# Optimization experiments

Hardware: AMD Instinct MI355X
Metric: run time of the kernel (lower is better)

## Reference

```python
import jax, jax.numpy as jnp
import numpy as np

B, SEQ, D_MODEL, N_HEADS = 4, 4096, 1024, 16
HEAD_DIM = D_MODEL // N_HEADS


def setup_inputs() -> dict:
    key = jax.random.key(0)
    ks = jax.random.split(key, 12)
    d = D_MODEL
    s = 1.0 / np.sqrt(d)  # ~nn.Linear init scale
    f = lambda k, shape, sc=1.0: jax.random.normal(k, shape, dtype=jnp.float32) * sc
    return {
        "queries": f(ks[0], (B, SEQ, d)),
        "keys":    f(ks[1], (B, SEQ, d)),
        "values":  f(ks[2], (B, SEQ, d)),
        "Wr": f(ks[3], (d, d), s), "br": jnp.zeros((d,), jnp.float32),
        "Wk": f(ks[4], (d, d), s), "bk": jnp.zeros((d,), jnp.float32),
        "Wv": f(ks[5], (d, d), s), "bv": jnp.zeros((d,), jnp.float32),
        "Wo": f(ks[6], (d, d), s), "bo": jnp.zeros((d,), jnp.float32),
        "decay": f(ks[7], (N_HEADS, HEAD_DIM), 0.01) - 5.0,
        "bonus": jnp.zeros((N_HEADS, HEAD_DIM), jnp.float32),
    }


def reference(queries, keys, values, Wr, br, Wk, bk, Wv, bv, Wo, bo, decay, bonus):
    Bb, N, d = queries.shape
    M = keys.shape[1]
    H = decay.shape[0]
    Dh = d // H

    # projections (nn.Linear: x @ W^T + b), split into heads
    r = (queries @ Wr.T + br).reshape(Bb, N, H, Dh)              # (B,N,H,D)
    k = (keys    @ Wk.T + bk).reshape(Bb, M, H, Dh).transpose(1, 0, 2, 3)  # (M,B,H,D)
    v = (values  @ Wv.T + bv).reshape(Bb, M, H, Dh).transpose(1, 0, 2, 3)  # (M,B,H,D)

    decay_factor = jnp.exp(-jnp.exp(decay))  # exp(w), w = -exp(decay); (H,D)

    def step(carry, kv):
        num, den = carry                       # (B,H,D)
        k_t, v_t = kv                          # (B,H,D)
        kc = jnp.clip(k_t, -10.0, 10.0)
        ek = jnp.exp(kc)
        bonus_w = jnp.exp(bonus + kc)          # (B,H,D) via broadcast
        wkv_t = (num + bonus_w * v_t) / (den + bonus_w + 1e-6)
        num = num * decay_factor + ek * v_t
        den = den * decay_factor + ek
        return (num, den), wkv_t

    init = (jnp.zeros((Bb, H, Dh), queries.dtype), jnp.zeros((Bb, H, Dh), queries.dtype))
    _, wkv = jax.lax.scan(step, init, (k, v))   # (M,B,H,D); here M == N
    wkv = wkv[:N].transpose(1, 0, 2, 3)         # (B,N,H,D)

    out = (jax.nn.sigmoid(r) * wkv).reshape(Bb, N, d)
    return out @ Wo.T + bo
```

## Files before the change

### kernel.cpp

```cpp
#include <hip/hip_runtime.h>

#define T_SEQ   4096
#define DM      1024
#define NB      4
#define ROWS    (NB * T_SEQ)
#define NCH     64
#define LCH     (T_SEQ / NCH)

typedef unsigned short ushort_t;

typedef __attribute__((ext_vector_type(8))) short bf16x8;
typedef __attribute__((ext_vector_type(4))) float f32x4;

__device__ __forceinline__ float bf2f(ushort_t u) {
  return __uint_as_float(((unsigned int)u) << 16);
}
__device__ __forceinline__ ushort_t f2bf(float f) {
  unsigned int u = __float_as_uint(f);
  u += 0x7FFFu + ((u >> 16) & 1u);
  return (ushort_t)(u >> 16);
}
__device__ __forceinline__ unsigned cvtpk(float lo, float hi) {
  unsigned r;
  asm("v_cvt_pk_bf16_f32 %0, %1, %2" : "=v"(r) : "v"(lo), "v"(hi));
  return r;
}

__device__ __forceinline__ void async16(const void* g, void* l) {
  __builtin_amdgcn_global_load_lds(
      (const __attribute__((address_space(1))) unsigned int*)g,
      (__attribute__((address_space(3))) unsigned int*)l, 16, 0, 0);
}

__device__ __forceinline__ int fragoff(int row, int col) {
  int p = (((row >> 4) * 2 + (col >> 5)) << 10) + ((row & 15) << 6) + ((col & 31) << 1);
  return p ^ (((row >> 3) & 1) << 5);
}
__device__ __forceinline__ int fragoffB32(int row, int col) {
  int p = ((row >> 4) << 10) + ((row & 15) << 6) + (col << 1);
  return p ^ (((row >> 3) & 1) << 5);
}
__device__ __forceinline__ int fragoffA32f(int row, int col) {
  int p = ((row >> 3) << 10) + ((row & 7) << 7) + (col << 2);
  return p ^ ((row & 7) << 4);
}

__global__ __launch_bounds__(256)
void cvt_pack(const float* __restrict__ Wr, const float* __restrict__ Wk,
              const float* __restrict__ Wv, const float* __restrict__ Wo,
              const float* __restrict__ br, const float* __restrict__ bk,
              const float* __restrict__ bv, const float* __restrict__ bo,
              ushort_t* __restrict__ wb, float* __restrict__ biasP) {
  const int bid = blockIdx.x;
  if (bid < 2048) {
    const int n4 = (DM * DM);
    for (int i = bid * 256 + threadIdx.x; i < n4; i += 2048 * 256) {
      const int seg = i >> 18;
      const float* src = seg == 0 ? Wr : seg == 1 ? Wk : seg == 2 ? Wv : Wo;
      const float4 f = ((const float4*)src)[i & 262143];
      ushort4 o;
      o.x = f2bf(f.x); o.y = f2bf(f.y); o.z = f2bf(f.z); o.w = f2bf(f.w);
      ((ushort4*)wb)[i] = o;
    }
  } else {
    const int s = bid - 2048;
    const float* b = s == 0 ? br : s == 1 ? bk : s == 2 ? bv : bo;
    for (int i = threadIdx.x; i < DM; i += 256) biasP[s * DM + i] = b[i];
  }
}

template <typename OutT>
__global__ __launch_bounds__(512, 2)
void gemm256(const ushort_t* __restrict__ A, const ushort_t* __restrict__ W,
             const float* __restrict__ bias, OutT* __restrict__ C,
             const int M, const int N, const int K) {
  __shared__ char smem[131072];
  const int T = K >> 6;
  const int nwg = (M >> 8) * (N >> 8);
  const int wg  = ((int)blockIdx.x & 7) * (nwg >> 3) + ((int)blockIdx.x >> 3);
  const int ntn = N >> 8;
  const int tm = wg / ntn, tn = wg % ntn;
  const int m0 = tm << 8, n0 = tn << 8;
  const int tid  = threadIdx.x;
  const int lane = tid & 63;
  const int wave = tid >> 6;
  const int wm128 = (wave >> 2) * 128;
  const int wn64  = (wave & 3) * 64;
  const int r15 = lane & 15;
  const int kq8 = (lane >> 4) * 8;

  int srow[2], scol[2];
  #pragma unroll
  for (int rho = 0; rho < 2; ++rho) {
    int p  = rho * 8192 + tid * 16;
    int pp = p ^ (((p >> 9) & 1) << 5);
    int e  = pp >> 1;
    int S = e >> 9, inr = e & 511;
    srow[rho] = ((S >> 1) << 4) + (inr >> 5);
    scol[rho] = ((S & 1) << 5) + (inr & 31);
  }

  auto stageA = [&](int tile, int half) {
    const int boff = ((tile & 1) << 15) + (half << 14);
    #pragma unroll
    for (int rho = 0; rho < 2; ++rho) {
      const ushort_t* g = A + (size_t)(m0 + half * 128 + srow[rho]) * K + (tile << 6) + scol[rho];
      async16(g, &smem[boff + rho * 8192 + tid * 16]);
    }
  };
  auto stageB = [&](int tile, int half) {
    const int boff = 65536 + ((tile & 1) << 15) + (half << 14);
    #pragma unroll
    for (int rho = 0; rho < 2; ++rho) {
      const ushort_t* g = W + (size_t)(n0 + half * 128 + srow[rho]) * K + (tile << 6) + scol[rho];
      async16(g, &smem[boff + rho * 8192 + tid * 16]);
    }
  };

  f32x4 acc[8][4];
  #pragma unroll
  for (int i = 0; i < 8; ++i)
    #pragma unroll
    for (int j = 0; j < 4; ++j)
      acc[i][j] = (f32x4){0.f, 0.f, 0.f, 0.f};
  bf16x8 bf[4][2];

  stageA(0, 0); stageA(0, 1); stageB(0, 0); stageB(0, 1); stageB(1, 0); stageB(1, 1);
  asm volatile("s_waitcnt vmcnt(4)" ::: "memory");
  __builtin_amdgcn_s_barrier();

#define GPHASE(Q, STG, TAILW)                                                    \
  {                                                                              \
    bf16x8 af[2][2];                                                             \
    _Pragma("unroll") for (int fl = 0; fl < 2; ++fl)                             \
      _Pragma("unroll") for (int ks = 0; ks < 2; ++ks)                           \
        af[fl][ks] = *(const bf16x8*)&smem[abase +                               \
            fragoff(wm128 + ((2 * (Q) + fl) << 4) + r15, (ks << 5) + kq8)];      \
    if ((Q) == 0) {                                                              \
      _Pragma("unroll") for (int fj = 0; fj < 4; ++fj)                           \
        _Pragma("unroll") for (int ks = 0; ks < 2; ++ks)                         \
          bf[fj][ks] = *(const bf16x8*)&smem[bbase +                             \
              fragoff(wn64 + (fj << 4) + r15, (ks << 5) + kq8)];                 \
    }                                                                            \
    STG();                                                                       \
    __builtin_amdgcn_s_barrier();                                                \
    __builtin_amdgcn_s_setprio(1);                                               \
    _Pragma("unroll") for (int fl = 0; fl < 2; ++fl)                             \
      _Pragma("unroll") for (int fj = 0; fj < 4; ++fj)                           \
        _Pragma("unroll") for (int ks = 0; ks < 2; ++ks)                         \
          acc[2 * (Q) + fl][fj] = __builtin_amdgcn_mfma_f32_16x16x32_bf16(       \
              af[fl][ks], bf[fj][ks], acc[2 * (Q) + fl][fj], 0, 0, 0);           \
    __builtin_amdgcn_s_setprio(0);                                               \
    TAILW();                                                                     \
    __builtin_amdgcn_s_barrier();                                                \
  }

  for (int j = 0; j < T; ++j) {
    const int abase = (j & 1) << 15;
    const int bbase = 65536 + ((j & 1) << 15);
    const bool p1 = (j + 1 < T), p2 = (j + 2 < T);
    auto s0 = [&] { if (p1) stageA(j + 1, 0); };
    auto s1 = [&] { if (p1) stageA(j + 1, 1); };
    auto s2 = [&] { if (p2) stageB(j + 2, 0); };
    auto s3 = [&] { if (p2) stageB(j + 2, 1); };
    auto nw = [&] {};
    auto bwait = [&] {
      if (p2) asm volatile("s_waitcnt vmcnt(4)" ::: "memory");
      else    asm volatile("s_waitcnt vmcnt(0)" ::: "memory");
    };
    GPHASE(0, s0, nw);
    GPHASE(1, s1, nw);
    GPHASE(2, s2, nw);
    GPHASE(3, s3, bwait);
  }
#undef GPHASE

  float bias4[4];
  #pragma unroll
  for (int fj = 0; fj < 4; ++fj) bias4[fj] = bias[n0 + wn64 + fj * 16 + r15];
  #pragma unroll
  for (int fi = 0; fi < 8; ++fi) {
    const int row0 = m0 + wm128 + fi * 16 + (lane >> 4) * 4;
    #pragma unroll
    for (int fj = 0; fj < 4; ++fj) {
      const int col = n0 + wn64 + fj * 16 + r15;
      #pragma unroll
      for (int r = 0; r < 4; ++r) {
        const float v = acc[fi][fj][r] + bias4[fj];
        if constexpr (sizeof(OutT) == 2) C[(size_t)(row0 + r) * N + col] = f2bf(v);
        else                             C[(size_t)(row0 + r) * N + col] = v;
      }
    }
  }
}

__global__ __launch_bounds__(512, 2)
void gemm256_proj(const float* __restrict__ Aq, const float* __restrict__ Ak,
                  const float* __restrict__ Av, const ushort_t* __restrict__ Wb,
                  const float* __restrict__ biasP, ushort_t* __restrict__ Cb,
                  const int M, const int N, const int K) {
  __shared__ char smem[98304];
  const int T = K >> 5;
  const int wg = ((int)blockIdx.x & 7) * 96 + ((int)blockIdx.x >> 3);
  const int g  = wg >> 8;
  const int local = wg & 255;
  const int ntn = N >> 8;
  const int tm = local / ntn, tn = local % ntn;
  const int m0 = tm << 8, n0 = tn << 8;
  const float*    Af = g == 0 ? Aq : (g == 1 ? Ak : Av);
  const ushort_t* W  = Wb + (size_t)g * N * K;
  const float*  bias = biasP + g * N;
  ushort_t*        C = Cb + (size_t)g * M * N;

  const int tid  = threadIdx.x;
  const int lane = tid & 63;
  const int wave = tid >> 6;
  const int wm128 = (wave >> 2) * 128;
  const int wn64  = (wave & 3) * 64;
  const int r15 = lane & 15;
  const int kq8 = (lane >> 4) * 8;

  int arow[2], acol[2];
  #pragma unroll
  for (int rho = 0; rho < 2; ++rho) {
    const int p = rho * 8192 + tid * 16;
    const int e = p ^ (((p >> 7) & 7) << 4);
    arow[rho] = ((p >> 10) << 3) | ((p >> 7) & 7);
    acol[rho] = (e >> 2) & 31;
  }
  int brow, bcol;
  {
    const int p = tid * 16;
    const int pp = p ^ (((p >> 9) & 1) << 5);
    const int e = pp >> 1;
    brow = ((e >> 9) << 4) | ((e >> 5) & 15);
    bcol = e & 31;
  }

  auto stageA = [&](int tile, int half) {
    const int boff = ((tile & 1) << 15) + (half << 14);
    #pragma unroll
    for (int rho = 0; rho < 2; ++rho) {
      const float* g2 = Af + (size_t)(m0 + half * 128 + arow[rho]) * K + (tile << 5) + acol[rho];
      async16(g2, &smem[boff + rho * 8192 + tid * 16]);
    }
  };
  auto stageB = [&](int tile, int half) {
    const int boff = 65536 + ((tile & 1) << 14) + (half << 13);
    const ushort_t* g2 = W + (size_t)(n0 + half * 128 + brow) * K + (tile << 5) + bcol;
    async16(g2, &smem[boff + tid * 16]);
  };

  auto rdA = [&](int abase, int row) -> bf16x8 {
    const int adlo = abase + fragoffA32f(row, kq8);
    const int adhi = abase + fragoffA32f(row, kq8 + 4);
    const f32x4 lo = *(const f32x4*)&smem[adlo];
    const f32x4 hi = *(const f32x4*)&smem[adhi];
    union { uint4 u4; bf16x8 b; } cv;
    cv.u4.x = cvtpk(lo[0], lo[1]); cv.u4.y = cvtpk(lo[2], lo[3]);
    cv.u4.z = cvtpk(hi[0], hi[1]); cv.u4.w = cvtpk(hi[2], hi[3]);
    return cv.b;
  };

  f32x4 acc[8][4];
  #pragma unroll
  for (int i = 0; i < 8; ++i)
    #pragma unroll
    for (int j = 0; j < 4; ++j)
      acc[i][j] = (f32x4){0.f, 0.f, 0.f, 0.f};
  bf16x8 bf[4];

  stageA(0, 0); stageA(0, 1); stageB(0, 0); stageB(0, 1); stageB(1, 0); stageB(1, 1);
  asm volatile("s_waitcnt vmcnt(2)" ::: "memory");
  __builtin_amdgcn_s_barrier();

#define PPHASE(Q, STG, TAILW)                                                    \
  {                                                                              \
    bf16x8 af[2];                                                                \
    _Pragma("unroll") for (int fl = 0; fl < 2; ++fl)                             \
      af[fl] = rdA(abase, wm128 + ((2 * (Q) + fl) << 4) + r15);                  \
    if ((Q) == 0) {                                                              \
      _Pragma("unroll") for (int fj = 0; fj < 4; ++fj)                           \
        bf[fj] = *(const bf16x8*)&smem[bbase +                                   \
            fragoffB32(wn64 + (fj << 4) + r15, kq8)];                            \
    }                                                                            \
    STG();                                                                       \
    __builtin_amdgcn_s_barrier();                                                \
    __builtin_amdgcn_s_setprio(1);                                               \
    _Pragma("unroll") for (int fl = 0; fl < 2; ++fl)                             \
      _Pragma("unroll") for (int fj = 0; fj < 4; ++fj)                           \
        acc[2 * (Q) + fl][fj] = __builtin_amdgcn_mfma_f32_16x16x32_bf16(         \
            af[fl], bf[fj], acc[2 * (Q) + fl][fj], 0, 0, 0);                     \
    __builtin_amdgcn_s_setprio(0);                                               \
    TAILW();                                                                     \
    __builtin_amdgcn_s_barrier();                                                \
  }

  for (int j = 0; j < T; ++j) {
    const int abase = (j & 1) << 15;
    const int bbase = 65536 + ((j & 1) << 14);
    const bool p1 = (j + 1 < T), p2 = (j + 2 < T);
    auto s0 = [&] { if (p1) stageA(j + 1, 0); };
    auto s1 = [&] { if (p1) stageA(j + 1, 1); };
    auto s2 = [&] { if (p2) { stageB(j + 2, 0); stageB(j + 2, 1); } };
    auto nw = [&] {};
    auto bwait = [&] {
      if (p2) asm volatile("s_waitcnt vmcnt(2)" ::: "memory");
      else    asm volatile("s_waitcnt vmcnt(0)" ::: "memory");
    };
    PPHASE(0, s0, nw);
    PPHASE(1, s1, nw);
    PPHASE(2, s2, nw);
    PPHASE(3, nw, bwait);
  }
#undef PPHASE

  float bias4[4];
  #pragma unroll
  for (int fj = 0; fj < 4; ++fj) bias4[fj] = bias[n0 + wn64 + fj * 16 + r15];
  #pragma unroll
  for (int fi = 0; fi < 8; ++fi) {
    const int row0 = m0 + wm128 + fi * 16 + (lane >> 4) * 4;
    #pragma unroll
    for (int fj = 0; fj < 4; ++fj) {
      const int col = n0 + wn64 + fj * 16 + r15;
      #pragma unroll
      for (int r = 0; r < 4; ++r)
        C[(size_t)(row0 + r) * N + col] = f2bf(acc[fi][fj][r] + bias4[fj]);
    }
  }
}

__global__ __launch_bounds__(256)
void wkv_pass1(const ushort_t* __restrict__ kp, const ushort_t* __restrict__ vp,
               const float* __restrict__ decay,
               float* __restrict__ s_num, float* __restrict__ s_den) {
  const int tid = threadIdx.x;
  const int grp = blockIdx.x & 3;
  const int c   = (blockIdx.x >> 2) & (NCH - 1);
  const int b   = (int)blockIdx.x >> 8;
  const int ch  = grp * 256 + tid;
  const float df = __expf(-__expf(decay[ch]));
  size_t idx = (size_t)b * T_SEQ * DM + (size_t)(c * LCH) * DM + ch;
  float num = 0.f, den = 0.f;
  for (int u = 0; u < LCH; ++u, idx += DM) {
    float kf = bf2f(kp[idx]);
    kf = fminf(fmaxf(kf, -10.f), 10.f);
    const float ek = __expf(kf);
    const float vv = bf2f(vp[idx]);
    num = fmaf(num, df, ek * vv);
    den = fmaf(den, df, ek);
  }
  const size_t si = ((size_t)b * NCH + c) * DM + ch;
  s_num[si] = num;
  s_den[si] = den;
}

__global__ __launch_bounds__(256)
void wkv_pass2(const float* __restrict__ decay,
               float* __restrict__ s_num, float* __restrict__ s_den) {
  const int tid = threadIdx.x;
  const int grp = blockIdx.x & 3;
  const int b   = (int)blockIdx.x >> 2;
  const int ch  = grp * 256 + tid;
  const float dfL = __expf(-__expf(decay[ch]) * (float)LCH);
  float an = 0.f, ad = 0.f;
  size_t si = (size_t)b * NCH * DM + ch;
  for (int c = 0; c < NCH; ++c, si += DM) {
    const float ln = s_num[si], ld = s_den[si];
    s_num[si] = an; s_den[si] = ad;
    an = fmaf(an, dfL, ln);
    ad = fmaf(ad, dfL, ld);
  }
}

__global__ __launch_bounds__(256)
void wkv_pass3(const ushort_t* __restrict__ kp, const ushort_t* __restrict__ vp,
               ushort_t* rg, const float* __restrict__ decay,
               const float* __restrict__ bonus,
               const float* __restrict__ s_num, const float* __restrict__ s_den) {
  const int tid = threadIdx.x;
  const int grp = blockIdx.x & 3;
  const int c   = (blockIdx.x >> 2) & (NCH - 1);
  const int b   = (int)blockIdx.x >> 8;
  const int ch  = grp * 256 + tid;
  const float df = __expf(-__expf(decay[ch]));
  const float eb = __expf(bonus[ch]);
  const size_t si = ((size_t)b * NCH + c) * DM + ch;
  float num = s_num[si], den = s_den[si];
  size_t idx = (size_t)b * T_SEQ * DM + (size_t)(c * LCH) * DM + ch;
  for (int u = 0; u < LCH; ++u, idx += DM) {
    float kf = bf2f(kp[idx]);
    kf = fminf(fmaxf(kf, -10.f), 10.f);
    const float ek = __expf(kf);
    const float bw = eb * ek;
    const float vv = bf2f(vp[idx]);
    const float rr = bf2f(rg[idx]);
    const float numer = fmaf(bw, vv, num);
    const float denom = den + bw + 1e-6f;
    const float wkv = numer * __builtin_amdgcn_rcpf(denom);
    const float sig = __builtin_amdgcn_rcpf(1.f + __expf(-rr));
    rg[idx] = f2bf(sig * wkv);
    num = fmaf(num, df, ek * vv);
    den = fmaf(den, df, ek);
  }
}

extern "C" void kernel_launch(void* const* d_in, const int* in_sizes, int n_in,
                              void* d_out, int out_size, void* d_ws, size_t ws_size,
                              hipStream_t stream) {
  const float* q   = (const float*)d_in[0];
  const float* ky  = (const float*)d_in[1];
  const float* vl  = (const float*)d_in[2];
  const float* Wr  = (const float*)d_in[3];
  const float* br  = (const float*)d_in[4];
  const float* Wk  = (const float*)d_in[5];
  const float* bk  = (const float*)d_in[6];
  const float* Wv  = (const float*)d_in[7];
  const float* bv  = (const float*)d_in[8];
  const float* Wo  = (const float*)d_in[9];
  const float* bo  = (const float*)d_in[10];
  const float* decay = (const float*)d_in[11];
  const float* bonus = (const float*)d_in[12];
  float* out = (float*)d_out;

  const size_t NE = (size_t)ROWS * DM;
  const size_t WE = (size_t)DM * DM;

  ushort_t* wb = (ushort_t*)d_ws;
  float* biasP = (float*)(wb + 4 * WE);
  ushort_t* rp = (ushort_t*)(biasP + 4 * DM);
  ushort_t* kp = rp + NE;
  ushort_t* vp = kp + NE;
  float* s_num = (float*)(vp + NE);
  float* s_den = s_num + (size_t)NB * NCH * DM;
  ushort_t* G  = rp;

  dim3 cB(256);
  dim3 gemmGrid((ROWS / 256) * (DM / 256)), gemmBlk(512);
  dim3 projGrid(3 * (ROWS / 256) * (DM / 256));
  dim3 scanGrid(NB * NCH * (DM / 256)), scanBlk(256);

  cvt_pack<<<dim3(2052), cB, 0, stream>>>(Wr, Wk, Wv, Wo, br, bk, bv, bo, wb, biasP);
  gemm256_proj<<<projGrid, gemmBlk, 0, stream>>>(q, ky, vl, wb, biasP, rp, ROWS, DM, DM);
  wkv_pass1<<<scanGrid, scanBlk, 0, stream>>>(kp, vp, decay, s_num, s_den);
  wkv_pass2<<<dim3(NB * DM / 256), scanBlk, 0, stream>>>(decay, s_num, s_den);
  wkv_pass3<<<scanGrid, scanBlk, 0, stream>>>(kp, vp, rp, decay, bonus, s_num, s_den);
  gemm256<float><<<gemmGrid, gemmBlk, 0, stream>>>(G, wb + 3 * WE, biasP + 3 * DM, out, ROWS, DM, DM);
}
```

Before: 258.8 us.

## Restructure projection GEMM with triple-buffered A and 64-wide K B tiles

```diff
diff --git a/kernel.cpp b/kernel.cpp
--- a/kernel.cpp
+++ b/kernel.cpp
@@ -35,14 +35,6 @@
 __device__ __forceinline__ int fragoff(int row, int col) {
   int p = (((row >> 4) * 2 + (col >> 5)) << 10) + ((row & 15) << 6) + ((col & 31) << 1);
   return p ^ (((row >> 3) & 1) << 5);
-}
-__device__ __forceinline__ int fragoffB32(int row, int col) {
-  int p = ((row >> 4) << 10) + ((row & 15) << 6) + (col << 1);
-  return p ^ (((row >> 3) & 1) << 5);
-}
-__device__ __forceinline__ int fragoffA32f(int row, int col) {
-  int p = ((row >> 3) << 10) + ((row & 7) << 7) + (col << 2);
-  return p ^ ((row & 7) << 4);
 }
 
 __global__ __launch_bounds__(256)
@@ -195,22 +187,24 @@
 }
 
 __global__ __launch_bounds__(512, 2)
-void gemm256_proj(const float* __restrict__ Aq, const float* __restrict__ Ak,
-                  const float* __restrict__ Av, const ushort_t* __restrict__ Wb,
-                  const float* __restrict__ biasP, ushort_t* __restrict__ Cb,
-                  const int M, const int N, const int K) {
-  __shared__ char smem[98304];
+void gemm3p(const float* __restrict__ Aq, const float* __restrict__ Ak,
+            const float* __restrict__ Av, const ushort_t* __restrict__ Wb,
+            const float* __restrict__ biasP, ushort_t* __restrict__ Cb,
+            const int M, const int N, const int K) {
+  __shared__ char smem[163840];
   const int T = K >> 5;
-  const int wg = ((int)blockIdx.x & 7) * 96 + ((int)blockIdx.x >> 3);
-  const int g  = wg >> 8;
-  const int local = wg & 255;
+  const int ntpg = (M >> 8) * (N >> 8);
+  const int nwg  = 3 * ntpg;
+  const int wg = ((int)blockIdx.x & 7) * (nwg >> 3) + ((int)blockIdx.x >> 3);
+  const int g     = wg / ntpg;
+  const int local = wg % ntpg;
   const int ntn = N >> 8;
   const int tm = local / ntn, tn = local % ntn;
   const int m0 = tm << 8, n0 = tn << 8;
-  const float*    Af = g == 0 ? Aq : (g == 1 ? Ak : Av);
-  const ushort_t* W  = Wb + (size_t)g * N * K;
-  const float*  bias = biasP + g * N;
-  ushort_t*        C = Cb + (size_t)g * M * N;
+  const float*    Af   = g == 0 ? Aq : (g == 1 ? Ak : Av);
+  const ushort_t* W    = Wb + (size_t)g * N * K;
+  const float*    bias = biasP + g * N;
+  ushort_t*       C    = Cb + (size_t)g * M * N;
 
   const int tid  = threadIdx.x;
   const int lane = tid & 63;
@@ -220,42 +214,47 @@
   const int r15 = lane & 15;
   const int kq8 = (lane >> 4) * 8;
 
-  int arow[2], acol[2];
+  int arow[4], acol[4];
+  #pragma unroll
+  for (int rho = 0; rho < 4; ++rho) {
+    const int p = (rho & 1) * 8192 + tid * 16;
+    const int e = (p ^ (((p >> 9) & 1) << 5)) >> 1;
+    const int S = e >> 9, inr = e & 511;
+    const int srl = ((S >> 1) << 4) + (inr >> 5);
+    const int E   = ((S & 1) << 5) + (inr & 31);
+    arow[rho] = (rho >> 1) * 128 + srl;
+    acol[rho] = ((E & 31) >> 3) * 8 + (E >> 5) * 4;
+  }
+  int brow[2], bcolE[2];
   #pragma unroll
   for (int rho = 0; rho < 2; ++rho) {
     const int p = rho * 8192 + tid * 16;
-    const int e = p ^ (((p >> 7) & 7) << 4);
-    arow[rho] = ((p >> 10) << 3) | ((p >> 7) & 7);
-    acol[rho] = (e >> 2) & 31;
-  }
-  int brow, bcol;
-  {
-    const int p = tid * 16;
-    const int pp = p ^ (((p >> 9) & 1) << 5);
-    const int e = pp >> 1;
-    brow = ((e >> 9) << 4) | ((e >> 5) & 15);
-    bcol = e & 31;
-  }
-
-  auto stageA = [&](int tile, int half) {
-    const int boff = ((tile & 1) << 15) + (half << 14);
+    const int e = (p ^ (((p >> 9) & 1) << 5)) >> 1;
+    const int S = e >> 9, inr = e & 511;
+    brow[rho]  = ((S >> 1) << 4) + (inr >> 5);
+    bcolE[rho] = ((S & 1) << 5) + (inr & 31);
+  }
+
+  auto stageA = [&](int tile) {
+    const int boff = (tile % 3) * 32768;
+    #pragma unroll
+    for (int rho = 0; rho < 4; ++rho) {
+      const float* s = Af + (size_t)(m0 + arow[rho]) * K + (tile << 5) + acol[rho];
+      async16(s, &smem[boff + (rho >> 1) * 16384 + (rho & 1) * 8192 + tid * 16]);
+    }
+  };
+  auto stageBh = [&](int bt, int half) {
+    const int boff = 98304 + (bt & 1) * 32768 + half * 16384;
     #pragma unroll
     for (int rho = 0; rho < 2; ++rho) {
-      const float* g2 = Af + (size_t)(m0 + half * 128 + arow[rho]) * K + (tile << 5) + acol[rho];
-      async16(g2, &smem[boff + rho * 8192 + tid * 16]);
+      const ushort_t* s = W + (size_t)(n0 + half * 128 + brow[rho]) * K + (bt << 6) + bcolE[rho];
+      async16(s, &smem[boff + rho * 8192 + tid * 16]);
     }
   };
-  auto stageB = [&](int tile, int half) {
-    const int boff = 65536 + ((tile & 1) << 14) + (half << 13);
-    const ushort_t* g2 = W + (size_t)(n0 + half * 128 + brow) * K + (tile << 5) + bcol;
-    async16(g2, &smem[boff + tid * 16]);
-  };
 
   auto rdA = [&](int abase, int row) -> bf16x8 {
-    const int adlo = abase + fragoffA32f(row, kq8);
-    const int adhi = abase + fragoffA32f(row, kq8 + 4);
-    const f32x4 lo = *(const f32x4*)&smem[adlo];
-    const f32x4 hi = *(const f32x4*)&smem[adhi];
+    const f32x4 lo = *(const f32x4*)&smem[abase + fragoff(row, kq8)];
+    const f32x4 hi = *(const f32x4*)&smem[abase + fragoff(row, kq8 + 32)];
     union { uint4 u4; bf16x8 b; } cv;
     cv.u4.x = cvtpk(lo[0], lo[1]); cv.u4.y = cvtpk(lo[2], lo[3]);
     cv.u4.z = cvtpk(hi[0], hi[1]); cv.u4.w = cvtpk(hi[2], hi[3]);
@@ -268,52 +267,58 @@
     #pragma unroll
     for (int j = 0; j < 4; ++j)
       acc[i][j] = (f32x4){0.f, 0.f, 0.f, 0.f};
-  bf16x8 bf[4];
-
-  stageA(0, 0); stageA(0, 1); stageB(0, 0); stageB(0, 1); stageB(1, 0); stageB(1, 1);
-  asm volatile("s_waitcnt vmcnt(2)" ::: "memory");
+  bf16x8 bfr[4];
+
+  stageA(0); stageBh(0, 0); stageBh(0, 1); stageA(1);
+  asm volatile("s_waitcnt vmcnt(4)" ::: "memory");
   __builtin_amdgcn_s_barrier();
 
-#define PPHASE(Q, STG, TAILW)                                                    \
-  {                                                                              \
-    bf16x8 af[2];                                                                \
-    _Pragma("unroll") for (int fl = 0; fl < 2; ++fl)                             \
-      af[fl] = rdA(abase, wm128 + ((2 * (Q) + fl) << 4) + r15);                  \
-    if ((Q) == 0) {                                                              \
-      _Pragma("unroll") for (int fj = 0; fj < 4; ++fj)                           \
-        bf[fj] = *(const bf16x8*)&smem[bbase +                                   \
-            fragoffB32(wn64 + (fj << 4) + r15, kq8)];                            \
-    }                                                                            \
-    STG();                                                                       \
-    __builtin_amdgcn_s_barrier();                                                \
-    __builtin_amdgcn_s_setprio(1);                                               \
-    _Pragma("unroll") for (int fl = 0; fl < 2; ++fl)                             \
-      _Pragma("unroll") for (int fj = 0; fj < 4; ++fj)                           \
-        acc[2 * (Q) + fl][fj] = __builtin_amdgcn_mfma_f32_16x16x32_bf16(         \
-            af[fl], bf[fj], acc[2 * (Q) + fl][fj], 0, 0, 0);                     \
-    __builtin_amdgcn_s_setprio(0);                                               \
-    TAILW();                                                                     \
-    __builtin_amdgcn_s_barrier();                                                \
-  }
-
   for (int j = 0; j < T; ++j) {
-    const int abase = (j & 1) << 15;
-    const int bbase = 65536 + ((j & 1) << 14);
-    const bool p1 = (j + 1 < T), p2 = (j + 2 < T);
-    auto s0 = [&] { if (p1) stageA(j + 1, 0); };
-    auto s1 = [&] { if (p1) stageA(j + 1, 1); };
-    auto s2 = [&] { if (p2) { stageB(j + 2, 0); stageB(j + 2, 1); } };
-    auto nw = [&] {};
-    auto bwait = [&] {
-      if (p2) asm volatile("s_waitcnt vmcnt(2)" ::: "memory");
-      else    asm volatile("s_waitcnt vmcnt(0)" ::: "memory");
-    };
-    PPHASE(0, s0, nw);
-    PPHASE(1, s1, nw);
-    PPHASE(2, s2, nw);
-    PPHASE(3, nw, bwait);
-  }
-#undef PPHASE
+    const int curA = (j % 3) * 32768;
+    const int curB = 98304 + ((j >> 1) & 1) * 32768;
+    const int ks   = (j & 1) << 5;
+    const bool pre  = (j + 2 < T);
+    const bool even = !(j & 1);
+    {
+      bf16x8 af[4];
+      #pragma unroll
+      for (int q = 0; q < 4; ++q) af[q] = rdA(curA, wm128 + q * 16 + r15);
+      #pragma unroll
+      for (int fj = 0; fj < 4; ++fj)
+        bfr[fj] = *(const bf16x8*)&smem[curB + fragoff(wn64 + (fj << 4) + r15, ks + kq8)];
+      if (pre) { stageA(j + 2); if (even) stageBh((j >> 1) + 1, 0); }
+      __builtin_amdgcn_s_barrier();
+      __builtin_amdgcn_s_setprio(1);
+      #pragma unroll
+      for (int q = 0; q < 4; ++q)
+        #pragma unroll
+        for (int fj = 0; fj < 4; ++fj)
+          acc[q][fj] = __builtin_amdgcn_mfma_f32_16x16x32_bf16(af[q], bfr[fj], acc[q][fj], 0, 0, 0);
+      __builtin_amdgcn_s_setprio(0);
+      __builtin_amdgcn_s_barrier();
+    }
+    {
+      bf16x8 af[4];
+      #pragma unroll
+      for (int q = 0; q < 4; ++q) af[q] = rdA(curA, wm128 + 64 + q * 16 + r15);
+      if (pre && even) stageBh((j >> 1) + 1, 1);
+      __builtin_amdgcn_s_barrier();
+      __builtin_amdgcn_s_setprio(1);
+      #pragma unroll
+      for (int q = 0; q < 4; ++q)
+        #pragma unroll
+        for (int fj = 0; fj < 4; ++fj)
+          acc[4 + q][fj] = __builtin_amdgcn_mfma_f32_16x16x32_bf16(af[q], bfr[fj], acc[4 + q][fj], 0, 0, 0);
+      __builtin_amdgcn_s_setprio(0);
+      if (pre) {
+        if (even) asm volatile("s_waitcnt vmcnt(8)" ::: "memory");
+        else      asm volatile("s_waitcnt vmcnt(4)" ::: "memory");
+      } else if (j + 1 < T) {
+        asm volatile("s_waitcnt vmcnt(0)" ::: "memory");
+      }
+      __builtin_amdgcn_s_barrier();
+    }
+  }
 
   float bias4[4];
   #pragma unroll
@@ -437,12 +442,13 @@
   ushort_t* G  = rp;
 
   dim3 cB(256);
-  dim3 gemmGrid((ROWS / 256) * (DM / 256)), gemmBlk(512);
+  dim3 gemmBlk(512);
   dim3 projGrid(3 * (ROWS / 256) * (DM / 256));
+  dim3 gemmGrid((ROWS / 256) * (DM / 256));
   dim3 scanGrid(NB * NCH * (DM / 256)), scanBlk(256);
 
   cvt_pack<<<dim3(2052), cB, 0, stream>>>(Wr, Wk, Wv, Wo, br, bk, bv, bo, wb, biasP);
-  gemm256_proj<<<projGrid, gemmBlk, 0, stream>>>(q, ky, vl, wb, biasP, rp, ROWS, DM, DM);
+  gemm3p<<<projGrid, gemmBlk, 0, stream>>>(q, ky, vl, wb, biasP, rp, ROWS, DM, DM);
   wkv_pass1<<<scanGrid, scanBlk, 0, stream>>>(kp, vp, decay, s_num, s_den);
   wkv_pass2<<<dim3(NB * DM / 256), scanBlk, 0, stream>>>(decay, s_num, s_den);
   wkv_pass3<<<scanGrid, scanBlk, 0, stream>>>(kp, vp, rp, decay, bonus, s_num, s_den);
```

Result: no change. 263.9 us (+2.0%).

## Stage fp32 activations through registers with bf16 conversion before LDS in projection GEMM

Applied to the files above, without the earlier changes.

```diff
diff --git a/kernel.cpp b/kernel.cpp
--- a/kernel.cpp
+++ b/kernel.cpp
@@ -35,14 +35,6 @@
 __device__ __forceinline__ int fragoff(int row, int col) {
   int p = (((row >> 4) * 2 + (col >> 5)) << 10) + ((row & 15) << 6) + ((col & 31) << 1);
   return p ^ (((row >> 3) & 1) << 5);
-}
-__device__ __forceinline__ int fragoffB32(int row, int col) {
-  int p = ((row >> 4) << 10) + ((row & 15) << 6) + (col << 1);
-  return p ^ (((row >> 3) & 1) << 5);
-}
-__device__ __forceinline__ int fragoffA32f(int row, int col) {
-  int p = ((row >> 3) << 10) + ((row & 7) << 7) + (col << 2);
-  return p ^ ((row & 7) << 4);
 }
 
 __global__ __launch_bounds__(256)
@@ -195,22 +187,24 @@
 }
 
 __global__ __launch_bounds__(512, 2)
-void gemm256_proj(const float* __restrict__ Aq, const float* __restrict__ Ak,
-                  const float* __restrict__ Av, const ushort_t* __restrict__ Wb,
-                  const float* __restrict__ biasP, ushort_t* __restrict__ Cb,
-                  const int M, const int N, const int K) {
-  __shared__ char smem[98304];
-  const int T = K >> 5;
-  const int wg = ((int)blockIdx.x & 7) * 96 + ((int)blockIdx.x >> 3);
-  const int g  = wg >> 8;
-  const int local = wg & 255;
+void gemm3r(const float* __restrict__ Aq, const float* __restrict__ Ak,
+            const float* __restrict__ Av, const ushort_t* __restrict__ Wb,
+            const float* __restrict__ biasP, ushort_t* __restrict__ Cb,
+            const int M, const int N, const int K) {
+  __shared__ char smem[131072];
+  const int T = K >> 6;
+  const int ntpg = (M >> 8) * (N >> 8);
+  const int nwg  = 3 * ntpg;
+  const int wg = ((int)blockIdx.x & 7) * (nwg >> 3) + ((int)blockIdx.x >> 3);
+  const int g     = wg / ntpg;
+  const int local = wg % ntpg;
   const int ntn = N >> 8;
   const int tm = local / ntn, tn = local % ntn;
   const int m0 = tm << 8, n0 = tn << 8;
-  const float*    Af = g == 0 ? Aq : (g == 1 ? Ak : Av);
-  const ushort_t* W  = Wb + (size_t)g * N * K;
-  const float*  bias = biasP + g * N;
-  ushort_t*        C = Cb + (size_t)g * M * N;
+  const float*    Af   = g == 0 ? Aq : (g == 1 ? Ak : Av);
+  const ushort_t* W    = Wb + (size_t)g * N * K;
+  const float*    bias = biasP + g * N;
+  ushort_t*       C    = Cb + (size_t)g * M * N;
 
   const int tid  = threadIdx.x;
   const int lane = tid & 63;
@@ -220,47 +214,50 @@
   const int r15 = lane & 15;
   const int kq8 = (lane >> 4) * 8;
 
-  int arow[2], acol[2];
+  int srow[2], scol[2];
   #pragma unroll
   for (int rho = 0; rho < 2; ++rho) {
-    const int p = rho * 8192 + tid * 16;
-    const int e = p ^ (((p >> 7) & 7) << 4);
-    arow[rho] = ((p >> 10) << 3) | ((p >> 7) & 7);
-    acol[rho] = (e >> 2) & 31;
-  }
-  int brow, bcol;
-  {
-    const int p = tid * 16;
-    const int pp = p ^ (((p >> 9) & 1) << 5);
-    const int e = pp >> 1;
-    brow = ((e >> 9) << 4) | ((e >> 5) & 15);
-    bcol = e & 31;
-  }
-
-  auto stageA = [&](int tile, int half) {
-    const int boff = ((tile & 1) << 15) + (half << 14);
+    int p  = rho * 8192 + tid * 16;
+    int pp = p ^ (((p >> 9) & 1) << 5);
+    int e  = pp >> 1;
+    int S = e >> 9, inr = e & 511;
+    srow[rho] = ((S >> 1) << 4) + (inr >> 5);
+    scol[rho] = ((S & 1) << 5) + (inr & 31);
+  }
+  int aRow[4], aCol[4];
+  #pragma unroll
+  for (int s = 0; s < 4; ++s) {
+    aRow[s] = (s >> 1) * 128 + srow[s & 1];
+    aCol[s] = scol[s & 1];
+  }
+
+  auto stageB = [&](int tile, int half) {
+    const int boff = 65536 + ((tile & 1) << 15) + (half << 14);
     #pragma unroll
     for (int rho = 0; rho < 2; ++rho) {
-      const float* g2 = Af + (size_t)(m0 + half * 128 + arow[rho]) * K + (tile << 5) + acol[rho];
-      async16(g2, &smem[boff + rho * 8192 + tid * 16]);
+      const ushort_t* gq = W + (size_t)(n0 + half * 128 + srow[rho]) * K + (tile << 6) + scol[rho];
+      async16(gq, &smem[boff + rho * 8192 + tid * 16]);
     }
   };
-  auto stageB = [&](int tile, int half) {
-    const int boff = 65536 + ((tile & 1) << 14) + (half << 13);
-    const ushort_t* g2 = W + (size_t)(n0 + half * 128 + brow) * K + (tile << 5) + bcol;
-    async16(g2, &smem[boff + tid * 16]);
-  };
-
-  auto rdA = [&](int abase, int row) -> bf16x8 {
-    const int adlo = abase + fragoffA32f(row, kq8);
-    const int adhi = abase + fragoffA32f(row, kq8 + 4);
-    const f32x4 lo = *(const f32x4*)&smem[adlo];
-    const f32x4 hi = *(const f32x4*)&smem[adhi];
-    union { uint4 u4; bf16x8 b; } cv;
-    cv.u4.x = cvtpk(lo[0], lo[1]); cv.u4.y = cvtpk(lo[2], lo[3]);
-    cv.u4.z = cvtpk(hi[0], hi[1]); cv.u4.w = cvtpk(hi[2], hi[3]);
-    return cv.b;
-  };
+
+  float4 regE[8], regO[8];
+
+#define ALOAD(DST, TILE)                                                         \
+  _Pragma("unroll") for (int s = 0; s < 4; ++s) {                                \
+    const float* src_ = Af + (size_t)(m0 + aRow[s]) * K + ((TILE) << 6) + aCol[s]; \
+    DST[2 * s]     = *(const float4*)src_;                                       \
+    DST[2 * s + 1] = *(const float4*)(src_ + 4);                                 \
+  }
+#define AWRITE2(SRC, TILE, S0)                                                   \
+  _Pragma("unroll") for (int s = (S0); s < (S0) + 2; ++s) {                      \
+    uint4 w_;                                                                    \
+    w_.x = cvtpk(SRC[2 * s][0], SRC[2 * s][1]);                                  \
+    w_.y = cvtpk(SRC[2 * s][2], SRC[2 * s][3]);                                  \
+    w_.z = cvtpk(SRC[2 * s + 1][0], SRC[2 * s + 1][1]);                          \
+    w_.w = cvtpk(SRC[2 * s + 1][2], SRC[2 * s + 1][3]);                          \
+    *(uint4*)&smem[(((TILE) & 1) << 15) + (s >> 1) * 16384 + (s & 1) * 8192 +    \
+                   tid * 16] = w_;                                               \
+  }
 
   f32x4 acc[8][4];
   #pragma unroll
@@ -268,52 +265,67 @@
     #pragma unroll
     for (int j = 0; j < 4; ++j)
       acc[i][j] = (f32x4){0.f, 0.f, 0.f, 0.f};
-  bf16x8 bf[4];
-
-  stageA(0, 0); stageA(0, 1); stageB(0, 0); stageB(0, 1); stageB(1, 0); stageB(1, 1);
-  asm volatile("s_waitcnt vmcnt(2)" ::: "memory");
+  bf16x8 bf[4][2];
+
+  ALOAD(regE, 0);
+  stageB(0, 0); stageB(0, 1);
+  ALOAD(regO, 1);
+  stageB(1, 0); stageB(1, 1);
+  AWRITE2(regE, 0, 0); AWRITE2(regE, 0, 2);
+  asm volatile("s_waitcnt vmcnt(12)" ::: "memory");
+  asm volatile("s_waitcnt lgkmcnt(0)" ::: "memory");
   __builtin_amdgcn_s_barrier();
 
-#define PPHASE(Q, STG, TAILW)                                                    \
+#define RPHASE(Q, STG, TAILW)                                                    \
   {                                                                              \
-    bf16x8 af[2];                                                                \
+    bf16x8 af[2][2];                                                             \
     _Pragma("unroll") for (int fl = 0; fl < 2; ++fl)                             \
-      af[fl] = rdA(abase, wm128 + ((2 * (Q) + fl) << 4) + r15);                  \
+      _Pragma("unroll") for (int ks = 0; ks < 2; ++ks)                           \
+        af[fl][ks] = *(const bf16x8*)&smem[abase +                               \
+            fragoff(wm128 + ((2 * (Q) + fl) << 4) + r15, (ks << 5) + kq8)];      \
     if ((Q) == 0) {                                                              \
       _Pragma("unroll") for (int fj = 0; fj < 4; ++fj)                           \
-        bf[fj] = *(const bf16x8*)&smem[bbase +                                   \
-            fragoffB32(wn64 + (fj << 4) + r15, kq8)];                            \
+        _Pragma("unroll") for (int ks = 0; ks < 2; ++ks)                         \
+          bf[fj][ks] = *(const bf16x8*)&smem[bbase +                             \
+              fragoff(wn64 + (fj << 4) + r15, (ks << 5) + kq8)];                 \
     }                                                                            \
-    STG();                                                                       \
+    STG                                                                          \
     __builtin_amdgcn_s_barrier();                                                \
     __builtin_amdgcn_s_setprio(1);                                               \
     _Pragma("unroll") for (int fl = 0; fl < 2; ++fl)                             \
       _Pragma("unroll") for (int fj = 0; fj < 4; ++fj)                           \
-        acc[2 * (Q) + fl][fj] = __builtin_amdgcn_mfma_f32_16x16x32_bf16(         \
-            af[fl], bf[fj], acc[2 * (Q) + fl][fj], 0, 0, 0);                     \
+        _Pragma("unroll") for (int ks = 0; ks < 2; ++ks)                         \
+          acc[2 * (Q) + fl][fj] = __builtin_amdgcn_mfma_f32_16x16x32_bf16(       \
+              af[fl][ks], bf[fj][ks], acc[2 * (Q) + fl][fj], 0, 0, 0);           \
     __builtin_amdgcn_s_setprio(0);                                               \
-    TAILW();                                                                     \
+    TAILW                                                                        \
     __builtin_amdgcn_s_barrier();                                                \
   }
 
-  for (int j = 0; j < T; ++j) {
-    const int abase = (j & 1) << 15;
-    const int bbase = 65536 + ((j & 1) << 14);
-    const bool p1 = (j + 1 < T), p2 = (j + 2 < T);
-    auto s0 = [&] { if (p1) stageA(j + 1, 0); };
-    auto s1 = [&] { if (p1) stageA(j + 1, 1); };
-    auto s2 = [&] { if (p2) { stageB(j + 2, 0); stageB(j + 2, 1); } };
-    auto nw = [&] {};
-    auto bwait = [&] {
-      if (p2) asm volatile("s_waitcnt vmcnt(2)" ::: "memory");
-      else    asm volatile("s_waitcnt vmcnt(0)" ::: "memory");
-    };
-    PPHASE(0, s0, nw);
-    PPHASE(1, s1, nw);
-    PPHASE(2, s2, nw);
-    PPHASE(3, nw, bwait);
-  }
-#undef PPHASE
+#define ITER(J, LD, CV)                                                          \
+  {                                                                              \
+    const int j_ = (J);                                                          \
+    const int abase = (j_ & 1) << 15;                                            \
+    const int bbase = 65536 + ((j_ & 1) << 15);                                  \
+    const bool pA = (j_ + 2 < T);                                                \
+    const bool pC = (j_ + 1 < T);                                                \
+    RPHASE(0, { if (pA) ALOAD(LD, j_ + 2); }, ;)                                 \
+    RPHASE(1, { if (pC) { AWRITE2(CV, j_ + 1, 0); } }, ;)                        \
+    RPHASE(2, { if (pA) stageB(j_ + 2, 0); if (pC) { AWRITE2(CV, j_ + 1, 2); } }, ;) \
+    RPHASE(3, { if (pA) stageB(j_ + 2, 1); },                                    \
+           { if (pA) asm volatile("s_waitcnt vmcnt(12)" ::: "memory");           \
+             else    asm volatile("s_waitcnt vmcnt(0)" ::: "memory");            \
+             asm volatile("s_waitcnt lgkmcnt(0)" ::: "memory"); })               \
+  }
+
+  for (int jj = 0; jj < T; jj += 2) {
+    ITER(jj,     regE, regO);
+    ITER(jj + 1, regO, regE);
+  }
+#undef ITER
+#undef RPHASE
+#undef ALOAD
+#undef AWRITE2
 
   float bias4[4];
   #pragma unroll
@@ -437,12 +449,12 @@
   ushort_t* G  = rp;
 
   dim3 cB(256);
-  dim3 gemmGrid((ROWS / 256) * (DM / 256)), gemmBlk(512);
-  dim3 projGrid(3 * (ROWS / 256) * (DM / 256));
+  dim3 projGrid(3 * (ROWS / 256) * (DM / 256)), gemmBlk(512);
+  dim3 gemmGrid((ROWS / 256) * (DM / 256));
   dim3 scanGrid(NB * NCH * (DM / 256)), scanBlk(256);
 
   cvt_pack<<<dim3(2052), cB, 0, stream>>>(Wr, Wk, Wv, Wo, br, bk, bv, bo, wb, biasP);
-  gemm256_proj<<<projGrid, gemmBlk, 0, stream>>>(q, ky, vl, wb, biasP, rp, ROWS, DM, DM);
+  gemm3r<<<projGrid, gemmBlk, 0, stream>>>(q, ky, vl, wb, biasP, rp, ROWS, DM, DM);
   wkv_pass1<<<scanGrid, scanBlk, 0, stream>>>(kp, vp, decay, s_num, s_den);
   wkv_pass2<<<dim3(NB * DM / 256), scanBlk, 0, stream>>>(decay, s_num, s_den);
   wkv_pass3<<<scanGrid, scanBlk, 0, stream>>>(kp, vp, rp, decay, bonus, s_num, s_den);
```

Result: slower. 518.4 us (+100.4%).
